# Optimization experiments

Hardware: AMD Instinct MI355X
Metric: run time of the kernel (lower is better)

## Reference

```python
import jax, jax.numpy as jnp
import numpy as np

N = 50000      # nodes
E = 800000     # edges (before self-loops)
F_IN = 256     # nfeat
HEADS = 8      # nhead
C1 = 16        # hidden_sizes (per-head channels of conv1)
NCLS = 40      # nclass
NEG_SLOPE = 0.2


def setup_inputs() -> dict:
    key = jax.random.key(0)
    ks = jax.random.split(key, 12)
    s = 0.1
    x = jax.random.normal(ks[0], (N, F_IN), dtype=jnp.float32)
    edge_index = jax.random.randint(ks[1], (2, E), 0, N, dtype=jnp.int64)
    edge_attr = jax.random.normal(ks[2], (E,), dtype=jnp.float32)  # unused by forward
    W1 = jax.random.normal(ks[3], (F_IN, HEADS * C1), dtype=jnp.float32) * s
    att_src1 = jax.random.normal(ks[4], (HEADS, C1), dtype=jnp.float32) * s
    att_dst1 = jax.random.normal(ks[5], (HEADS, C1), dtype=jnp.float32) * s
    b1 = jnp.zeros((HEADS * C1,), dtype=jnp.float32)
    W2 = jax.random.normal(ks[6], (HEADS * C1, NCLS), dtype=jnp.float32) * s
    att_src2 = jax.random.normal(ks[7], (1, NCLS), dtype=jnp.float32) * s
    att_dst2 = jax.random.normal(ks[8], (1, NCLS), dtype=jnp.float32) * s
    b2 = jnp.zeros((NCLS,), dtype=jnp.float32)
    return {"x": x, "edge_index": edge_index, "edge_attr": edge_attr,
            "W1": W1, "att_src1": att_src1, "att_dst1": att_dst1, "b1": b1,
            "W2": W2, "att_src2": att_src2, "att_dst2": att_dst2, "b2": b2}


def gat_layer(x, W, att_src, att_dst, bias, src, dst, concat):
    """PyG-style GATConv (eval mode, no dropout). src/dst include self-loops."""
    H, C = att_src.shape
    h = (x @ W).reshape(-1, H, C)                     # [N,H,C]
    a_src = (h * att_src[None]).sum(-1)               # [N,H]
    a_dst = (h * att_dst[None]).sum(-1)               # [N,H]
    e = jax.nn.leaky_relu(a_src[src] + a_dst[dst], NEG_SLOPE)  # [Etot,H]
    # segment softmax over destination neighborhoods
    m = jax.ops.segment_max(e, dst, num_segments=N)   # [N,H]
    m = jax.lax.stop_gradient(jnp.where(jnp.isfinite(m), m, 0.0))
    p = jnp.exp(e - m[dst])
    denom = jax.ops.segment_sum(p, dst, num_segments=N)
    alpha = p / (denom[dst] + 1e-16)                  # [Etot,H]
    out = jax.ops.segment_sum(alpha[:, :, None] * h[src], dst, num_segments=N)  # [N,H,C]
    out = out.reshape(-1, H * C) if concat else out.mean(axis=1)
    return out + bias


def reference(x, edge_index, edge_attr, W1, att_src1, att_dst1, b1, W2, att_src2, att_dst2, b2):
    # add self loops (PyG GATConv default)
    loops = jnp.arange(N, dtype=edge_index.dtype)
    src = jnp.concatenate([edge_index[0], loops])
    dst = jnp.concatenate([edge_index[1], loops])
    # eval mode: F.dropout is identity
    h = jax.nn.elu(gat_layer(x, W1, att_src1, att_dst1, b1, src, dst, concat=True))
    final = gat_layer(h, W2, att_src2, att_dst2, b2, src, dst, concat=False)
    return final, jax.nn.log_softmax(final, axis=1)
```

## Files before the change

### kernel.cpp

```cpp
#include <hip/hip_runtime.h>

#define NN 50000
#define EE 800000
#define FIN 256
#define HD 8
#define C1 16
#define HC 128
#define NC 40
#define NEG 0.2f
#define CAP 64
#define R2 32
#define BM 64
#define GB1 ((NN + BM - 1) / BM)
#define NP_N (NN / 8)
#define SCB 2048

typedef __attribute__((ext_vector_type(8))) short short8;
typedef __attribute__((ext_vector_type(4))) float f32x4;
union FragU { uint4 u; short8 s; };

__device__ __forceinline__ float leaky(float v){ return v > 0.f ? v : NEG * v; }

__device__ __forceinline__ unsigned int f2bf(float f){
  unsigned int u = __float_as_uint(f);
  u += 0x7fffu + ((u >> 16) & 1u);
  return u >> 16;
}
__device__ __forceinline__ unsigned int pack2bf(float a, float b){
  return f2bf(a) | (f2bf(b) << 16);
}
__device__ __forceinline__ float bflo(unsigned int u){ return __uint_as_float(u << 16); }
__device__ __forceinline__ float bfhi(unsigned int u){ return __uint_as_float(u & 0xffff0000u); }
__device__ __forceinline__ float bfus(unsigned short u){ return __uint_as_float((unsigned int)u << 16); }

__global__ __launch_bounds__(256) void k_prep(const float* __restrict__ W1,
                                              uint4* __restrict__ W1bfs){
  int f = blockIdx.x * 256 + threadIdx.x;
  int lane = f & 63, nt = (f >> 6) & 7, kt = f >> 9;
  int quad = lane >> 4, l16 = lane & 15;
  const float* src = W1 + (size_t)(kt * 32 + quad * 8) * HC + nt * 16 + l16;
  unsigned int p[4];
#pragma unroll
  for (int jj = 0; jj < 4; jj++){
    float v0 = src[(size_t)(2 * jj) * HC];
    float v1 = src[(size_t)(2 * jj + 1) * HC];
    p[jj] = pack2bf(v0, v1);
  }
  W1bfs[f] = make_uint4(p[0], p[1], p[2], p[3]);
}

__global__ __launch_bounds__(256, 3) void k_gemm1(const float* __restrict__ x,
                                                  const uint4* __restrict__ W1bfs,
                                                  const float* __restrict__ att_s,
                                                  const float* __restrict__ att_d,
                                                  const int* __restrict__ ei,
                                                  unsigned short* __restrict__ h1b,
                                                  float* __restrict__ as1,
                                                  float* __restrict__ ad1,
                                                  int* __restrict__ cnt,
                                                  int* __restrict__ srcp){
  const int tid = threadIdx.x;
  if (blockIdx.x >= GB1){
    const int part = blockIdx.x & 7, rank = (blockIdx.x - GB1) >> 3;
    const int lo = part * NP_N, hi = lo + NP_N;
    for (int e = rank * 256 + tid; e < EE; e += 256 * 256){
      int d = ei[EE + e];
      if (d >= lo && d < hi){
        int s = ei[e];
        int pos = atomicAdd(&cnt[d], 1);
        if (pos < CAP) srcp[d * CAP + pos] = s;
      }
    }
    return;
  }
  const int wave = tid >> 6, lane = tid & 63;
  const int quad = lane >> 4, l16 = lane & 15;
  const int m0 = blockIdx.x * BM + wave * 16;
  int arow = m0 + l16; if (arow >= NN) arow = NN - 1;
  const float* xr = x + (size_t)arow * FIN;

  float4 xa[16];
#pragma unroll
  for (int kt = 0; kt < 8; kt++){
    xa[2 * kt]     = *(const float4*)(xr + kt * 32 + quad * 8);
    xa[2 * kt + 1] = *(const float4*)(xr + kt * 32 + quad * 8 + 4);
  }
  FragU bf[8];
#pragma unroll
  for (int nt = 0; nt < 8; nt++) bf[nt].u = W1bfs[nt * 64 + lane];

  f32x4 acc[8];
#pragma unroll
  for (int t = 0; t < 8; t++) acc[t] = (f32x4){0.f, 0.f, 0.f, 0.f};

#pragma unroll
  for (int kt = 0; kt < 8; kt++){
    FragU bn[8];
    if (kt < 7){
#pragma unroll
      for (int nt = 0; nt < 8; nt++)
        bn[nt].u = W1bfs[((kt + 1) * 8 + nt) * 64 + lane];
    }
    FragU af;
    af.u = make_uint4(pack2bf(xa[2 * kt].x,     xa[2 * kt].y),
                      pack2bf(xa[2 * kt].z,     xa[2 * kt].w),
                      pack2bf(xa[2 * kt + 1].x, xa[2 * kt + 1].y),
                      pack2bf(xa[2 * kt + 1].z, xa[2 * kt + 1].w));
#pragma unroll
    for (int nt = 0; nt < 8; nt++)
      acc[nt] = __builtin_amdgcn_mfma_f32_16x16x32_bf16(af.s, bf[nt].s, acc[nt], 0, 0, 0);
    if (kt < 7){
#pragma unroll
      for (int nt = 0; nt < 8; nt++) bf[nt] = bn[nt];
    }
  }

  float sv[8], dv[8];
#pragma unroll
  for (int h = 0; h < 8; h++){ sv[h] = att_s[h * 16 + l16]; dv[h] = att_d[h * 16 + l16]; }
#pragma unroll
  for (int r = 0; r < 4; r++){
    const int gr = m0 + quad * 4 + r;
    float s[8], d[8];
#pragma unroll
    for (int h = 0; h < 8; h++){ s[h] = acc[h][r] * sv[h]; d[h] = acc[h][r] * dv[h]; }
#pragma unroll
    for (int o = 1; o < 16; o <<= 1){
#pragma unroll
      for (int h = 0; h < 8; h++){ s[h] += __shfl_xor(s[h], o); d[h] += __shfl_xor(d[h], o); }
    }
    if (gr < NN){
#pragma unroll
      for (int h = 0; h < 8; h++)
        h1b[(size_t)gr * HC + h * 16 + l16] = (unsigned short)f2bf(acc[h][r]);
      if (l16 == 0){
        *(float4*)(as1 + gr * 8)     = make_float4(s[0], s[1], s[2], s[3]);
        *(float4*)(as1 + gr * 8 + 4) = make_float4(s[4], s[5], s[6], s[7]);
        *(float4*)(ad1 + gr * 8)     = make_float4(d[0], d[1], d[2], d[3]);
        *(float4*)(ad1 + gr * 8 + 4) = make_float4(d[4], d[5], d[6], d[7]);
      }
    }
  }
}

__global__ __launch_bounds__(512) void k_agg1(const int* __restrict__ srcp,
                                              const int* __restrict__ cnt,
                                              const float* __restrict__ as1,
                                              const float* __restrict__ ad1,
                                              const unsigned short* __restrict__ h1b,
                                              const float* __restrict__ b1,
                                              unsigned short* __restrict__ h2b){
  __shared__ float wls[8][64][8];
  __shared__ int   sls[8][64];
  const int lane = threadIdx.x & 63, w = threadIdx.x >> 6;
  const int n = blockIdx.x * 8 + w;
  int deg = cnt[n]; if (deg > CAP - 1) deg = CAP - 1;
  const int nE = deg + 1;
  int sA = n;
  if (lane < deg) sA = srcp[n * CAP + lane];
  sls[w][lane] = sA << 6;

  const int h = lane >> 3, e8 = lane & 7;
  const float adg = ad1[n * 8 + h];
  int nCh = (nE + 7) >> 3; if (nCh < 2) nCh = 2;

  float mx = -3.0e38f;
  for (int c = 0; c < nCh; c++){
    const int i = c * 8 + e8;
    const int s8 = sls[w][i] >> 3;
    const float v = (i < nE) ? leaky(as1[(size_t)(unsigned)(s8 + h)] + adg) : -3.0e38f;
    wls[w][i][h] = v;
    mx = fmaxf(mx, v);
  }
  mx = fmaxf(mx, __shfl_xor(mx, 1));
  mx = fmaxf(mx, __shfl_xor(mx, 2));
  mx = fmaxf(mx, __shfl_xor(mx, 4));

  float den = 0.f;
  for (int c = 0; c < nCh; c++){
    const int i = c * 8 + e8;
    const float v = wls[w][i][h];
    const float wt = (i < nE) ? __expf(v - mx) : 0.f;
    wls[w][i][h] = wt;
    den += wt;
  }
  den += __shfl_xor(den, 1);
  den += __shfl_xor(den, 2);
  den += __shfl_xor(den, 4);

  const unsigned int* hp = (const unsigned int*)h1b;
  float ax = 0.f, ay = 0.f;
  {
    unsigned int u[16]; float q[16];
#pragma unroll
    for (int i = 0; i < 16; i++){
      u[i] = hp[(size_t)(unsigned)(sls[w][i] + lane)];
      q[i] = wls[w][i][h];
    }
#pragma unroll
    for (int i = 0; i < 16; i++){ ax += q[i] * bflo(u[i]); ay += q[i] * bfhi(u[i]); }
  }
  for (int i0 = 16; i0 < nE; i0 += 8){
    unsigned int uu[8]; float qq[8];
#pragma unroll
    for (int t = 0; t < 8; t++){
      const int j = i0 + t;
      uu[t] = hp[(size_t)(unsigned)(sls[w][j] + lane)];
      qq[t] = (j < nE) ? wls[w][j][h] : 0.f;
    }
#pragma unroll
    for (int t = 0; t < 8; t++){ ax += qq[t] * bflo(uu[t]); ay += qq[t] * bfhi(uu[t]); }
  }

  const float invd = 1.f / (den + 1e-16f);
  const float2 bb = *(const float2*)(b1 + 2 * lane);
  float ox = ax * invd + bb.x;
  float oy = ay * invd + bb.y;
  ox = ox > 0.f ? ox : (__expf(ox) - 1.f);
  oy = oy > 0.f ? oy : (__expf(oy) - 1.f);
  *(unsigned int*)(h2b + (size_t)n * HC + 2 * lane) = pack2bf(ox, oy);
}

__global__ __launch_bounds__(256) void k_gemm2(const unsigned short* __restrict__ h2b,
                                               const float* __restrict__ W2,
                                               const float* __restrict__ att_s2,
                                               const float* __restrict__ att_d2,
                                               unsigned short* __restrict__ gb,
                                               float* __restrict__ as2,
                                               float* __restrict__ ad2){
  __shared__ float hs[R2][HC + 2];
  __shared__ float w2s[HC * NC];
  const int tid = threadIdx.x;
  const int r0 = blockIdx.x * R2;
  for (int i = tid; i < HC * NC; i += 256) w2s[i] = W2[i];
  for (int i = tid; i < R2 * (HC / 2); i += 256){
    int r = i / (HC / 2), c = i % (HC / 2);
    unsigned int u = (r0 + r < NN) ? ((const unsigned int*)h2b)[(size_t)(r0 + r) * (HC / 2) + c] : 0u;
    hs[r][2 * c]     = bflo(u);
    hs[r][2 * c + 1] = bfhi(u);
  }
  __syncthreads();
  const int r = tid >> 3, j = tid & 7;
  float acc[5] = {0.f, 0.f, 0.f, 0.f, 0.f};
  for (int k = 0; k < HC; k++){
    float hv = hs[r][k];
#pragma unroll
    for (int q = 0; q < 5; q++) acc[q] += hv * w2s[k * NC + j + 8 * q];
  }
  const int node = r0 + r;
  if (node < NN){
    float s = 0.f, d = 0.f;
#pragma unroll
    for (int q = 0; q < 5; q++){
      int c = j + 8 * q;
      gb[(size_t)node * NC + c] = (unsigned short)f2bf(acc[q]);
      s += acc[q] * att_s2[c];
      d += acc[q] * att_d2[c];
    }
#pragma unroll
    for (int o = 1; o < 8; o <<= 1){ s += __shfl_xor(s, o); d += __shfl_xor(d, o); }
    if (j == 0){ as2[node] = s; ad2[node] = d; }
  }
}

__global__ __launch_bounds__(512) void k_agg2(const int* __restrict__ srcp,
                                              const int* __restrict__ cnt,
                                              const float* __restrict__ as2,
                                              const float* __restrict__ ad2,
                                              const unsigned short* __restrict__ gb,
                                              const float* __restrict__ b2,
                                              float* __restrict__ out){
  __shared__ float wls[8][64];
  __shared__ int   sls[8][64];
  const int lane = threadIdx.x & 63, w = threadIdx.x >> 6;
  const int n = blockIdx.x * 8 + w;
  int deg = cnt[n]; if (deg > CAP - 1) deg = CAP - 1;
  const int nE = deg + 1;
  const bool act = (lane <= deg);
  int sA = n;
  if (lane < deg) sA = srcp[n * CAP + lane];
  const float ad = ad2[n];
  float v = act ? leaky(as2[sA] + ad) : -3.0e38f;
  sls[w][lane] = sA * NC;
  float mx = v;
#pragma unroll
  for (int o = 1; o < 64; o <<= 1) mx = fmaxf(mx, __shfl_xor(mx, o));
  float wt = act ? __expf(v - mx) : 0.f;
  float den = wt;
#pragma unroll
  for (int o = 1; o < 64; o <<= 1) den += __shfl_xor(den, o);
  wls[w][lane] = wt;

  const int c = min(lane, NC - 1);
  float acc = 0.f;
  {
    float g[16], q[16];
#pragma unroll
    for (int i = 0; i < 16; i++){
      g[i] = bfus(gb[(size_t)(unsigned)(sls[w][i] + c)]);
      q[i] = wls[w][i];
    }
#pragma unroll
    for (int i = 0; i < 16; i++) acc += q[i] * g[i];
  }
  for (int i0 = 16; i0 < nE; i0 += 8){
    float gg[8], qq[8];
#pragma unroll
    for (int t = 0; t < 8; t++){
      const int j = i0 + t;
      gg[t] = bfus(gb[(size_t)(unsigned)(sls[w][j] + c)]);
      qq[t] = wls[w][j];
    }
#pragma unroll
    for (int t = 0; t < 8; t++) acc += qq[t] * gg[t];
  }
  const float invd = 1.f / (den + 1e-16f);
  const bool cl = (lane < NC);
  float f = acc * invd + b2[c];
  if (cl) out[(size_t)n * NC + lane] = f;
  float fv = cl ? f : -3.4e38f;
  float m2 = fv;
#pragma unroll
  for (int o = 1; o < 64; o <<= 1) m2 = fmaxf(m2, __shfl_xor(m2, o));
  float ex = cl ? __expf(fv - m2) : 0.f;
#pragma unroll
  for (int o = 1; o < 64; o <<= 1) ex += __shfl_xor(ex, o);
  const float lse = m2 + __logf(ex);
  if (cl) out[(size_t)(NN * NC) + (size_t)n * NC + lane] = fv - lse;
}

extern "C" void kernel_launch(void* const* d_in, const int* in_sizes, int n_in,
                              void* d_out, int out_size, void* d_ws, size_t ws_size,
                              hipStream_t stream){
  const float* x      = (const float*)d_in[0];
  const int*   ei     = (const int*)  d_in[1];
  const float* W1     = (const float*)d_in[3];
  const float* att_s1 = (const float*)d_in[4];
  const float* att_d1 = (const float*)d_in[5];
  const float* b1     = (const float*)d_in[6];
  const float* W2     = (const float*)d_in[7];
  const float* att_s2 = (const float*)d_in[8];
  const float* att_d2 = (const float*)d_in[9];
  const float* b2     = (const float*)d_in[10];
  float* out = (float*)d_out;

  char* wp = (char*)d_ws;
  uint4* W1bfs = (uint4*)wp;                 wp += (size_t)4096 * 16;
  unsigned short* h1b = (unsigned short*)wp; wp += (size_t)NN * HC * 2;
  unsigned short* h2b = (unsigned short*)wp; wp += (size_t)NN * HC * 2;
  unsigned short* gb  = (unsigned short*)wp; wp += (size_t)NN * NC * 2;
  float* as1 = (float*)wp;                   wp += (size_t)NN * HD * 4;
  float* ad1 = (float*)wp;                   wp += (size_t)NN * HD * 4;
  float* as2 = (float*)wp;                   wp += (size_t)NN * 4;
  float* ad2 = (float*)wp;                   wp += (size_t)NN * 4;
  int* cnt   = (int*)wp;                     wp += (size_t)NN * 4;
  int* srcp  = (int*)wp;                     wp += (size_t)NN * CAP * 4;

  hipMemsetAsync(cnt, 0, (size_t)NN * sizeof(int), stream);
  k_prep  <<<16, 256, 0, stream>>>(W1, W1bfs);
  k_gemm1 <<<GB1 + SCB, 256, 0, stream>>>(x, W1bfs, att_s1, att_d1, ei, h1b, as1, ad1, cnt, srcp);
  k_agg1  <<<NN / 8, 512, 0, stream>>>(srcp, cnt, as1, ad1, h1b, b1, h2b);
  k_gemm2 <<<(NN + R2 - 1) / R2, 256, 0, stream>>>(h2b, W2, att_s2, att_d2, gb, as2, ad2);
  k_agg2  <<<NN / 8, 512, 0, stream>>>(srcp, cnt, as2, ad2, gb, b2, out);
}
```

Before: 254.4 us.

## Use MFMA for second GEMM, stage GEMM1 inputs via LDS, move CSR build

The second layer's fp32 scalar LDS GEMM becomes a bf16 MFMA kernel whose weights are pre-packed into fragments by the prep kernel. GEMM1 now loads x into a swizzled LDS tile with global_load_lds instead of direct register loads. The edge-bucketing work moves from the GEMM1 launch into the prep launch, so the GEMM1 blocks no longer share a launch with atomic scatter blocks. The trade-off is more LDS use per GEMM1 block (64 KB, occupancy bound lowered to 2) and an edge scatter that now runs serially before GEMM1 instead of alongside it.

```diff
diff --git a/kernel.cpp b/kernel.cpp
--- a/kernel.cpp
+++ b/kernel.cpp
@@ -9,11 +9,12 @@
 #define NC 40
 #define NEG 0.2f
 #define CAP 64
-#define R2 32
 #define BM 64
+#define BM2 64
 #define GB1 ((NN + BM - 1) / BM)
 #define NP_N (NN / 8)
 #define SCB 2048
+#define PREPB 19
 
 typedef __attribute__((ext_vector_type(8))) short short8;
 typedef __attribute__((ext_vector_type(4))) float f32x4;
@@ -33,66 +34,96 @@
 __device__ __forceinline__ float bfhi(unsigned int u){ return __uint_as_float(u & 0xffff0000u); }
 __device__ __forceinline__ float bfus(unsigned short u){ return __uint_as_float((unsigned int)u << 16); }
 
+__device__ __forceinline__ void gld_lds16(const void* g, void* l){
+  __builtin_amdgcn_global_load_lds((const __attribute__((address_space(1))) unsigned int*)g,
+                                   (__attribute__((address_space(3))) unsigned int*)l,
+                                   16, 0, 0);
+}
+
 __global__ __launch_bounds__(256) void k_prep(const float* __restrict__ W1,
-                                              uint4* __restrict__ W1bfs){
-  int f = blockIdx.x * 256 + threadIdx.x;
-  int lane = f & 63, nt = (f >> 6) & 7, kt = f >> 9;
-  int quad = lane >> 4, l16 = lane & 15;
-  const float* src = W1 + (size_t)(kt * 32 + quad * 8) * HC + nt * 16 + l16;
-  unsigned int p[4];
-#pragma unroll
-  for (int jj = 0; jj < 4; jj++){
-    float v0 = src[(size_t)(2 * jj) * HC];
-    float v1 = src[(size_t)(2 * jj + 1) * HC];
-    p[jj] = pack2bf(v0, v1);
-  }
-  W1bfs[f] = make_uint4(p[0], p[1], p[2], p[3]);
-}
-
-__global__ __launch_bounds__(256, 3) void k_gemm1(const float* __restrict__ x,
+                                              uint4* __restrict__ W1bfs,
+                                              const float* __restrict__ W2,
+                                              uint4* __restrict__ W2bfs,
+                                              const int* __restrict__ ei,
+                                              int* __restrict__ cnt,
+                                              int* __restrict__ srcp){
+  const int tid = threadIdx.x;
+  if (blockIdx.x < 16){
+    int f = blockIdx.x * 256 + tid;
+    int lane = f & 63, nt = (f >> 6) & 7, kt = f >> 9;
+    int quad = lane >> 4, l16 = lane & 15;
+    const float* src = W1 + (size_t)(kt * 32 + quad * 8) * HC + nt * 16 + l16;
+    unsigned int p[4];
+#pragma unroll
+    for (int jj = 0; jj < 4; jj++)
+      p[jj] = pack2bf(src[(size_t)(2 * jj) * HC], src[(size_t)(2 * jj + 1) * HC]);
+    W1bfs[f] = make_uint4(p[0], p[1], p[2], p[3]);
+    return;
+  }
+  if (blockIdx.x < PREPB){
+    int f = (blockIdx.x - 16) * 256 + tid;
+    int lane = f & 63, frag = f >> 6;
+    int kt = frag / 3, nt = frag - kt * 3;
+    int quad = lane >> 4, l16 = lane & 15;
+    int n = nt * 16 + l16;
+    int k0 = kt * 32 + quad * 8;
+    unsigned int p[4];
+#pragma unroll
+    for (int jj = 0; jj < 4; jj++){
+      float v0 = (n < NC) ? W2[(size_t)(k0 + 2 * jj) * NC + n] : 0.f;
+      float v1 = (n < NC) ? W2[(size_t)(k0 + 2 * jj + 1) * NC + n] : 0.f;
+      p[jj] = pack2bf(v0, v1);
+    }
+    W2bfs[f] = make_uint4(p[0], p[1], p[2], p[3]);
+    return;
+  }
+  const int b = blockIdx.x - PREPB;
+  const int part = b & 7, rank = b >> 3;
+  const int lo = part * NP_N, hi = lo + NP_N;
+  for (int e = rank * 256 + tid; e < EE; e += 256 * 256){
+    int d = ei[EE + e];
+    if (d >= lo && d < hi){
+      int s = ei[e];
+      int pos = atomicAdd(&cnt[d], 1);
+      if (pos < CAP) srcp[d * CAP + pos] = s;
+    }
+  }
+}
+
+__global__ __launch_bounds__(256, 2) void k_gemm1(const float* __restrict__ x,
                                                   const uint4* __restrict__ W1bfs,
                                                   const float* __restrict__ att_s,
                                                   const float* __restrict__ att_d,
-                                                  const int* __restrict__ ei,
                                                   unsigned short* __restrict__ h1b,
                                                   float* __restrict__ as1,
-                                                  float* __restrict__ ad1,
-                                                  int* __restrict__ cnt,
-                                                  int* __restrict__ srcp){
+                                                  float* __restrict__ ad1){
+  __shared__ float xs[BM * FIN];
   const int tid = threadIdx.x;
-  if (blockIdx.x >= GB1){
-    const int part = blockIdx.x & 7, rank = (blockIdx.x - GB1) >> 3;
-    const int lo = part * NP_N, hi = lo + NP_N;
-    for (int e = rank * 256 + tid; e < EE; e += 256 * 256){
-      int d = ei[EE + e];
-      if (d >= lo && d < hi){
-        int s = ei[e];
-        int pos = atomicAdd(&cnt[d], 1);
-        if (pos < CAP) srcp[d * CAP + pos] = s;
-      }
-    }
-    return;
-  }
   const int wave = tid >> 6, lane = tid & 63;
   const int quad = lane >> 4, l16 = lane & 15;
-  const int m0 = blockIdx.x * BM + wave * 16;
-  int arow = m0 + l16; if (arow >= NN) arow = NN - 1;
-  const float* xr = x + (size_t)arow * FIN;
-
-  float4 xa[16];
-#pragma unroll
-  for (int kt = 0; kt < 8; kt++){
-    xa[2 * kt]     = *(const float4*)(xr + kt * 32 + quad * 8);
-    xa[2 * kt + 1] = *(const float4*)(xr + kt * 32 + quad * 8 + 4);
-  }
+  const int m0 = blockIdx.x * BM;
+  const int wr0 = wave * 16;
+
+#pragma unroll
+  for (int i = 0; i < 16; i++){
+    int grow = m0 + wr0 + i; if (grow >= NN) grow = NN - 1;
+    const float* src = x + (size_t)grow * FIN + ((lane ^ (i & 7)) << 2);
+    gld_lds16(src, &xs[(wr0 + i) * FIN]);
+  }
+
   FragU bf[8];
 #pragma unroll
   for (int nt = 0; nt < 8; nt++) bf[nt].u = W1bfs[nt * 64 + lane];
 
+  asm volatile("s_waitcnt vmcnt(0)" ::: "memory");
+  __builtin_amdgcn_sched_barrier(0);
+
   f32x4 acc[8];
 #pragma unroll
   for (int t = 0; t < 8; t++) acc[t] = (f32x4){0.f, 0.f, 0.f, 0.f};
 
+  const int swz = l16 & 7;
+  const float* xrow = &xs[(wr0 + l16) * FIN];
 #pragma unroll
   for (int kt = 0; kt < 8; kt++){
     FragU bn[8];
@@ -101,11 +132,12 @@
       for (int nt = 0; nt < 8; nt++)
         bn[nt].u = W1bfs[((kt + 1) * 8 + nt) * 64 + lane];
     }
+    const int g0 = kt * 8 + quad * 2;
+    const float4 a0 = *(const float4*)(xrow + ((g0 ^ swz) << 2));
+    const float4 a1 = *(const float4*)(xrow + (((g0 + 1) ^ swz) << 2));
     FragU af;
-    af.u = make_uint4(pack2bf(xa[2 * kt].x,     xa[2 * kt].y),
-                      pack2bf(xa[2 * kt].z,     xa[2 * kt].w),
-                      pack2bf(xa[2 * kt + 1].x, xa[2 * kt + 1].y),
-                      pack2bf(xa[2 * kt + 1].z, xa[2 * kt + 1].w));
+    af.u = make_uint4(pack2bf(a0.x, a0.y), pack2bf(a0.z, a0.w),
+                      pack2bf(a1.x, a1.y), pack2bf(a1.z, a1.w));
 #pragma unroll
     for (int nt = 0; nt < 8; nt++)
       acc[nt] = __builtin_amdgcn_mfma_f32_16x16x32_bf16(af.s, bf[nt].s, acc[nt], 0, 0, 0);
@@ -120,7 +152,7 @@
   for (int h = 0; h < 8; h++){ sv[h] = att_s[h * 16 + l16]; dv[h] = att_d[h * 16 + l16]; }
 #pragma unroll
   for (int r = 0; r < 4; r++){
-    const int gr = m0 + quad * 4 + r;
+    const int gr = m0 + wr0 + quad * 4 + r;
     float s[8], d[8];
 #pragma unroll
     for (int h = 0; h < 8; h++){ s[h] = acc[h][r] * sv[h]; d[h] = acc[h][r] * dv[h]; }
@@ -221,45 +253,73 @@
   *(unsigned int*)(h2b + (size_t)n * HC + 2 * lane) = pack2bf(ox, oy);
 }
 
-__global__ __launch_bounds__(256) void k_gemm2(const unsigned short* __restrict__ h2b,
-                                               const float* __restrict__ W2,
-                                               const float* __restrict__ att_s2,
-                                               const float* __restrict__ att_d2,
-                                               unsigned short* __restrict__ gb,
-                                               float* __restrict__ as2,
-                                               float* __restrict__ ad2){
-  __shared__ float hs[R2][HC + 2];
-  __shared__ float w2s[HC * NC];
+__global__ __launch_bounds__(256, 3) void k_gemm2(const unsigned short* __restrict__ h2b,
+                                                  const uint4* __restrict__ W2bfs,
+                                                  const float* __restrict__ att_s2,
+                                                  const float* __restrict__ att_d2,
+                                                  unsigned short* __restrict__ gb,
+                                                  float* __restrict__ as2,
+                                                  float* __restrict__ ad2){
+  __shared__ unsigned short h2s[BM2 * HC];
   const int tid = threadIdx.x;
-  const int r0 = blockIdx.x * R2;
-  for (int i = tid; i < HC * NC; i += 256) w2s[i] = W2[i];
-  for (int i = tid; i < R2 * (HC / 2); i += 256){
-    int r = i / (HC / 2), c = i % (HC / 2);
-    unsigned int u = (r0 + r < NN) ? ((const unsigned int*)h2b)[(size_t)(r0 + r) * (HC / 2) + c] : 0u;
-    hs[r][2 * c]     = bflo(u);
-    hs[r][2 * c + 1] = bfhi(u);
-  }
-  __syncthreads();
-  const int r = tid >> 3, j = tid & 7;
-  float acc[5] = {0.f, 0.f, 0.f, 0.f, 0.f};
-  for (int k = 0; k < HC; k++){
-    float hv = hs[r][k];
-#pragma unroll
-    for (int q = 0; q < 5; q++) acc[q] += hv * w2s[k * NC + j + 8 * q];
-  }
-  const int node = r0 + r;
-  if (node < NN){
-    float s = 0.f, d = 0.f;
-#pragma unroll
-    for (int q = 0; q < 5; q++){
-      int c = j + 8 * q;
-      gb[(size_t)node * NC + c] = (unsigned short)f2bf(acc[q]);
-      s += acc[q] * att_s2[c];
-      d += acc[q] * att_d2[c];
-    }
-#pragma unroll
-    for (int o = 1; o < 8; o <<= 1){ s += __shfl_xor(s, o); d += __shfl_xor(d, o); }
-    if (j == 0){ as2[node] = s; ad2[node] = d; }
+  const int wave = tid >> 6, lane = tid & 63;
+  const int quad = lane >> 4, l16 = lane & 15;
+  const int m0 = blockIdx.x * BM2;
+  const int wr0 = wave * 16;
+
+#pragma unroll
+  for (int i = 0; i < 4; i++){
+    const int rl = i * 4 + (lane >> 4);
+    int grow = m0 + wr0 + rl; if (grow >= NN) grow = NN - 1;
+    const int g = lane & 15;
+    const unsigned short* src = h2b + (size_t)grow * HC + ((g ^ (rl & 7)) << 3);
+    gld_lds16(src, &h2s[(wr0 + i * 4) * HC]);
+  }
+
+  FragU b2f[12];
+#pragma unroll
+  for (int f = 0; f < 12; f++) b2f[f].u = W2bfs[f * 64 + lane];
+
+  asm volatile("s_waitcnt vmcnt(0)" ::: "memory");
+  __builtin_amdgcn_sched_barrier(0);
+
+  f32x4 acc[3];
+#pragma unroll
+  for (int t = 0; t < 3; t++) acc[t] = (f32x4){0.f, 0.f, 0.f, 0.f};
+
+  const int swz = l16 & 7;
+  const unsigned short* hrow = &h2s[(wr0 + l16) * HC];
+#pragma unroll
+  for (int kt = 0; kt < 4; kt++){
+    FragU af;
+    af.u = *(const uint4*)(hrow + (((kt * 4 + quad) ^ swz) << 3));
+#pragma unroll
+    for (int nt = 0; nt < 3; nt++)
+      acc[nt] = __builtin_amdgcn_mfma_f32_16x16x32_bf16(af.s, b2f[kt * 3 + nt].s, acc[nt], 0, 0, 0);
+  }
+
+  float sv[3], dv[3];
+#pragma unroll
+  for (int nt = 0; nt < 3; nt++){
+    const int c = nt * 16 + l16;
+    sv[nt] = (c < NC) ? att_s2[c] : 0.f;
+    dv[nt] = (c < NC) ? att_d2[c] : 0.f;
+  }
+#pragma unroll
+  for (int r = 0; r < 4; r++){
+    const int gr = m0 + wr0 + quad * 4 + r;
+    float s = acc[0][r] * sv[0] + acc[1][r] * sv[1] + acc[2][r] * sv[2];
+    float d = acc[0][r] * dv[0] + acc[1][r] * dv[1] + acc[2][r] * dv[2];
+#pragma unroll
+    for (int o = 1; o < 16; o <<= 1){ s += __shfl_xor(s, o); d += __shfl_xor(d, o); }
+    if (gr < NN){
+#pragma unroll
+      for (int nt = 0; nt < 3; nt++){
+        const int c = nt * 16 + l16;
+        if (c < NC) gb[(size_t)gr * NC + c] = (unsigned short)f2bf(acc[nt][r]);
+      }
+      if (l16 == 0){ as2[gr] = s; ad2[gr] = d; }
+    }
   }
 }
 
@@ -346,6 +406,7 @@
 
   char* wp = (char*)d_ws;
   uint4* W1bfs = (uint4*)wp;                 wp += (size_t)4096 * 16;
+  uint4* W2bfs = (uint4*)wp;                 wp += (size_t)768 * 16;
   unsigned short* h1b = (unsigned short*)wp; wp += (size_t)NN * HC * 2;
   unsigned short* h2b = (unsigned short*)wp; wp += (size_t)NN * HC * 2;
   unsigned short* gb  = (unsigned short*)wp; wp += (size_t)NN * NC * 2;
@@ -357,9 +418,9 @@
   int* srcp  = (int*)wp;                     wp += (size_t)NN * CAP * 4;
 
   hipMemsetAsync(cnt, 0, (size_t)NN * sizeof(int), stream);
-  k_prep  <<<16, 256, 0, stream>>>(W1, W1bfs);
-  k_gemm1 <<<GB1 + SCB, 256, 0, stream>>>(x, W1bfs, att_s1, att_d1, ei, h1b, as1, ad1, cnt, srcp);
+  k_prep  <<<PREPB + SCB, 256, 0, stream>>>(W1, W1bfs, W2, W2bfs, ei, cnt, srcp);
+  k_gemm1 <<<GB1, 256, 0, stream>>>(x, W1bfs, att_s1, att_d1, h1b, as1, ad1);
   k_agg1  <<<NN / 8, 512, 0, stream>>>(srcp, cnt, as1, ad1, h1b, b1, h2b);
-  k_gemm2 <<<(NN + R2 - 1) / R2, 256, 0, stream>>>(h2b, W2, att_s2, att_d2, gb, as2, ad2);
+  k_gemm2 <<<(NN + BM2 - 1) / BM2, 256, 0, stream>>>(h2b, W2bfs, att_s2, att_d2, gb, as2, ad2);
   k_agg2  <<<NN / 8, 512, 0, stream>>>(srcp, cnt, as2, ad2, gb, b2, out);
 }
```

Result: faster. 238.2 us (-6.3%).
